# Performance work log

Hardware: AMD Instinct MI355X
Metric: run time of the kernel (lower is better)

## Reference

```python
import jax, jax.numpy as jnp
import numpy as np

B, T, H, K = 4, 1024, 1024, 16
HD = H // K  # head dim
EPS = 1e-5


def _layernorm(x, g, b):
    mu = jnp.mean(x, axis=-1, keepdims=True)
    var = jnp.mean(jnp.square(x - mu), axis=-1, keepdims=True)
    return (x - mu) * jax.lax.rsqrt(var + EPS) * g + b


def setup_inputs() -> dict:
    key = jax.random.key(0)
    ks = jax.random.split(key, 16)
    s = 0.02
    return {
        "x": jax.random.normal(ks[0], (B, T, H), jnp.float32),
        "ln1_g": jnp.ones((H,), jnp.float32),
        "ln1_b": jnp.zeros((H,), jnp.float32),
        "ln2_g": jnp.ones((H,), jnp.float32),
        "ln2_b": jnp.zeros((H,), jnp.float32),
        "Wq": jax.random.normal(ks[1], (H, H), jnp.float32) * s,
        "bq": jnp.zeros((H,), jnp.float32),
        "Wk": jax.random.normal(ks[2], (H, H), jnp.float32) * s,
        "bk": jnp.zeros((H,), jnp.float32),
        "Wv": jax.random.normal(ks[3], (H, H), jnp.float32) * s,
        "bv": jnp.zeros((H,), jnp.float32),
        "W1": jax.random.normal(ks[4], (H, 4 * H), jnp.float32) * s,
        "b1": jnp.zeros((4 * H,), jnp.float32),
        "W2": jax.random.normal(ks[5], (4 * H, H), jnp.float32) * s,
        "b2": jnp.zeros((H,), jnp.float32),
    }


def reference(x, ln1_g, ln1_b, ln2_g, ln2_b, Wq, bq, Wk, bk, Wv, bv, W1, b1, W2, b2):
    # --- attention sub-block ---
    h = _layernorm(x, ln1_g, ln1_b)                      # (B,T,H)
    q = (h @ Wq + bq).reshape(B, T, K, HD).transpose(0, 2, 1, 3)  # (B,K,T,hd)
    k = (h @ Wk + bk).reshape(B, T, K, HD).transpose(0, 2, 1, 3)
    v = (h @ Wv + bv).reshape(B, T, K, HD).transpose(0, 2, 1, 3)
    qkt = jnp.einsum('bkqd,bkpd->bkqp', q, k)            # (B,K,T,T)
    attn = qkt * (1.0 / np.sqrt(HD))
    # module quirk: masked positions are FILLED with 1e-9 (not -inf) before softmax
    causal_mask = jnp.triu(jnp.ones((T, T), bool), k=1)  # True above diagonal = masked
    attn = jnp.where(causal_mask, jnp.float32(1e-9), attn)
    attn = jax.nn.softmax(attn, axis=-1)
    y = jnp.einsum('bkqp,bkpd->bkqd', attn, v)           # (B,K,T,hd)
    y = y.transpose(0, 2, 1, 3).reshape(B, T, H)
    x = x + y
    # --- MLP sub-block (dropout is identity at eval) ---
    h2 = _layernorm(x, ln2_g, ln2_b)
    m = jax.nn.gelu(h2 @ W1 + b1, approximate=False) @ W2 + b2
    return x + m
```

## Files before the change

kernel.cpp:

```cpp
#include <hip/hip_runtime.h>
#include <hip/hip_bf16.h>
#include <math.h>


typedef __attribute__((ext_vector_type(8))) short bf16x8;
typedef __attribute__((ext_vector_type(4))) float f32x4;

#define DEVINL __device__ __forceinline__

#define LOG2E_SCALE 0.18033688f
#define MASK2 1.4426950408889634e-9f

DEVINL void stage16(const __hip_bfloat16* g, short* l) {
  __builtin_amdgcn_global_load_lds(
      (const __attribute__((address_space(1))) unsigned int*)g,
      (__attribute__((address_space(3))) unsigned int*)l, 16, 0, 0);
}

DEVINL float bf2f(short u) {
  unsigned x = ((unsigned)(unsigned short)u) << 16;
  float f; __builtin_memcpy(&f, &x, 4); return f;
}

DEVINL short f2bf_s(float f) {
  __hip_bfloat16 h = __float2bfloat16(f);
  short s; __builtin_memcpy(&s, &h, 2); return s;
}

DEVINL float block_sum(float v, float* sb) {
  #pragma unroll
  for (int o = 32; o; o >>= 1) v += __shfl_down(v, o);
  const int lane = threadIdx.x & 63, w = threadIdx.x >> 6;
  if (lane == 0) sb[w] = v;
  __syncthreads();
  float r = sb[0] + sb[1] + sb[2] + sb[3];
  __syncthreads();
  return r;
}

template<int BM, int BN, int WM, int WN>
DEVINL void gemm_core64(const __hip_bfloat16* __restrict__ A, int lda,
                        const __hip_bfloat16* __restrict__ Bt, int ldb,
                        int Kd, int row0, int col0,
                        f32x4 (&acc)[WM/16][WN/16],
                        short* lds_a, short* lds_b) {
  constexpr int MI = WM / 16, NI = WN / 16, WNC = BN / WN;
  constexpr int CA = BM * 8, CB = BN * 8;
  const int tid = threadIdx.x;
  const int lane = tid & 63, wave = tid >> 6;
  const int wm = (wave / WNC) * WM, wn = (wave % WNC) * WN;
  const int lr = lane & 15, lq = lane >> 4;
  for (int k0 = 0; k0 < Kd; k0 += 64) {
    #pragma unroll
    for (int c = tid; c < CA; c += 256) {
      const int r = c >> 3, kc = ((c & 7) ^ (r & 7)) << 3;
      stage16(A + (size_t)(row0 + r) * lda + k0 + kc, lds_a + c * 8);
    }
    #pragma unroll
    for (int c = tid; c < CB; c += 256) {
      const int r = c >> 3, kc = ((c & 7) ^ (r & 7)) << 3;
      stage16(Bt + (size_t)(col0 + r) * ldb + k0 + kc, lds_b + c * 8);
    }
    __syncthreads();
    #pragma unroll
    for (int s = 0; s < 2; s++) {
      bf16x8 af[MI], bfr[NI];
      #pragma unroll
      for (int mi = 0; mi < MI; mi++) {
        const int m = wm + mi * 16 + lr;
        af[mi] = *(const bf16x8*)(lds_a + m * 64 + (((s * 4 + lq) ^ (m & 7)) << 3));
      }
      #pragma unroll
      for (int ni = 0; ni < NI; ni++) {
        const int n = wn + ni * 16 + lr;
        bfr[ni] = *(const bf16x8*)(lds_b + n * 64 + (((s * 4 + lq) ^ (n & 7)) << 3));
      }
      #pragma unroll
      for (int mi = 0; mi < MI; mi++)
        #pragma unroll
        for (int ni = 0; ni < NI; ni++)
          acc[mi][ni] = __builtin_amdgcn_mfma_f32_16x16x32_bf16(
              af[mi], bfr[ni], acc[mi][ni], 0, 0, 0);
    }
    __syncthreads();
  }
}

__global__ __launch_bounds__(256) void k_tcvt(const float* __restrict__ src,
                                              __hip_bfloat16* __restrict__ dst,
                                              int R, int C, int dstOff, int dstPitch) {
  __shared__ float tile[32][33];
  const int c0 = blockIdx.x * 32, r0 = blockIdx.y * 32;
  const int tx = threadIdx.x, ty = threadIdx.y;
  #pragma unroll
  for (int i = 0; i < 32; i += 8)
    tile[ty + i][tx] = src[(size_t)(r0 + ty + i) * C + c0 + tx];
  __syncthreads();
  #pragma unroll
  for (int i = 0; i < 32; i += 8)
    dst[(size_t)(c0 + ty + i + dstOff) * dstPitch + r0 + tx] =
        __float2bfloat16(tile[tx][ty + i]);
}

__global__ __launch_bounds__(256) void k_tcvt3(const float* __restrict__ Wq,
                                               const float* __restrict__ Wk,
                                               const float* __restrict__ Wv,
                                               __hip_bfloat16* __restrict__ dst) {
  __shared__ float tile[32][33];
  const float* src = blockIdx.z == 0 ? Wq : (blockIdx.z == 1 ? Wk : Wv);
  const int dstOff = blockIdx.z << 10;
  const int c0 = blockIdx.x * 32, r0 = blockIdx.y * 32;
  const int tx = threadIdx.x, ty = threadIdx.y;
  #pragma unroll
  for (int i = 0; i < 32; i += 8)
    tile[ty + i][tx] = src[(size_t)(r0 + ty + i) * 1024 + c0 + tx];
  __syncthreads();
  #pragma unroll
  for (int i = 0; i < 32; i += 8)
    dst[(size_t)(c0 + ty + i + dstOff) * 1024 + r0 + tx] =
        __float2bfloat16(tile[tx][ty + i]);
}

__global__ __launch_bounds__(256) void k_pack_bias(const float* __restrict__ bq,
                                                   const float* __restrict__ bk,
                                                   const float* __restrict__ bv,
                                                   float* __restrict__ o) {
  const int i = blockIdx.x * 256 + threadIdx.x;
  if (i < 3072)
    o[i] = i < 1024 ? bq[i] : (i < 2048 ? bk[i - 1024] : bv[i - 2048]);
}

__global__ __launch_bounds__(256) void k_ln(const float* __restrict__ x,
                                            const float* __restrict__ y,
                                            const float* __restrict__ g,
                                            const float* __restrict__ bb,
                                            __hip_bfloat16* __restrict__ o,
                                            const float* __restrict__ badd,
                                            float* __restrict__ oinit) {
  __shared__ float sb[4];
  const int t = threadIdx.x;
  const size_t base = (size_t)blockIdx.x * 1024 + t * 4;
  const int c = t * 4;
  float4 xv = *(const float4*)(x + base);
  if (y) {
    float4 yv = *(const float4*)(y + base);
    xv.x += yv.x; xv.y += yv.y; xv.z += yv.z; xv.w += yv.w;
    float4 ov;
    ov.x = xv.x + badd[c + 0]; ov.y = xv.y + badd[c + 1];
    ov.z = xv.z + badd[c + 2]; ov.w = xv.w + badd[c + 3];
    *(float4*)(oinit + base) = ov;
  }
  const float mu = block_sum(xv.x + xv.y + xv.z + xv.w, sb) * (1.f / 1024.f);
  const float dx = xv.x - mu, dy = xv.y - mu, dz = xv.z - mu, dw = xv.w - mu;
  const float var = block_sum(dx * dx + dy * dy + dz * dz + dw * dw, sb) * (1.f / 1024.f);
  const float rs = rsqrtf(var + 1e-5f);
  o[base + 0] = __float2bfloat16(dx * rs * g[c + 0] + bb[c + 0]);
  o[base + 1] = __float2bfloat16(dy * rs * g[c + 1] + bb[c + 1]);
  o[base + 2] = __float2bfloat16(dz * rs * g[c + 2] + bb[c + 2]);
  o[base + 3] = __float2bfloat16(dw * rs * g[c + 3] + bb[c + 3]);
}

__global__ __launch_bounds__(256) void k_gemm_qkv(
    const __hip_bfloat16* __restrict__ h1, const __hip_bfloat16* __restrict__ Wt,
    const float* __restrict__ bqkv, __hip_bfloat16* __restrict__ Q,
    __hip_bfloat16* __restrict__ K, __hip_bfloat16* __restrict__ Vt) {
  __shared__ alignas(16) short smem[16896];
  short* la = smem;
  short* lb = smem + 8192;
  short* lc = smem;
  const int row0 = blockIdx.x * 128, col0 = blockIdx.y * 128;
  f32x4 acc[4][4] = {};
  gemm_core64<128, 128, 64, 64>(h1, 1024, Wt, 1024, 1024, row0, col0, acc, la, lb);
  const int tid = threadIdx.x, lane = tid & 63, wave = tid >> 6;
  const int wm = (wave >> 1) * 64, wn = (wave & 1) * 64, lr = lane & 15, lq = lane >> 4;
  const int which = col0 >> 10;
  const int h0 = (col0 & 1023) >> 6;
  const int b = row0 >> 10, t0 = row0 & 1023;
  if (which < 2) {
    const float qs = (which == 0) ? LOG2E_SCALE : 1.f;
    #pragma unroll
    for (int mi = 0; mi < 4; mi++)
      #pragma unroll
      for (int ni = 0; ni < 4; ni++)
        #pragma unroll
        for (int r = 0; r < 4; r++) {
          const int row = wm + mi * 16 + lq * 4 + r;
          const int col = wn + ni * 16 + lr;
          lc[row * 132 + col] = f2bf_s((acc[mi][ni][r] + bqkv[col0 + col]) * qs);
        }
    __syncthreads();
    __hip_bfloat16* O = which == 0 ? Q : K;
    #pragma unroll
    for (int c = 0; c < 8; c++) {
      const int f = tid + 256 * c;
      const int r = f >> 4, cc = f & 15;
      const int col = cc * 8;
      const int head = h0 + (col >> 6), d = col & 63;
      float4 vv = *(const float4*)(lc + r * 132 + col);
      *(float4*)(O + (((size_t)(b * 16 + head)) << 16) + (t0 + r) * 64 + d) = vv;
    }
  } else {
    #pragma unroll
    for (int mi = 0; mi < 4; mi++)
      #pragma unroll
      for (int ni = 0; ni < 4; ni++)
        #pragma unroll
        for (int r = 0; r < 4; r++) {
          const int row = wm + mi * 16 + lq * 4 + r;
          const int col = wn + ni * 16 + lr;
          lc[col * 132 + row] = f2bf_s(acc[mi][ni][r] + bqkv[col0 + col]);
        }
    __syncthreads();
    #pragma unroll
    for (int c = 0; c < 8; c++) {
      const int f = tid + 256 * c;
      const int dl = f >> 4, tc = f & 15;
      const int head = h0 + (dl >> 6), d = dl & 63;
      float4 vv = *(const float4*)(lc + dl * 132 + tc * 8);
      *(float4*)(Vt + (((size_t)(b * 16 + head)) << 16) + (size_t)d * 1024 +
                 t0 + tc * 8) = vv;
    }
  }
}

__global__ __launch_bounds__(256) void k_tailv(const __hip_bfloat16* __restrict__ Vt,
                                               float* __restrict__ TV) {
  __shared__ float ts[8][64];
  const int hb = blockIdx.x, tid = threadIdx.x;
  const __hip_bfloat16* Vh = Vt + ((size_t)hb << 16);
  for (int w = tid; w < 512; w += 256) {
    const int kt = w >> 6, d = w & 63;
    const short* p = (const short*)(Vh + (size_t)d * 1024 + kt * 128);
    float s = 0.f;
    for (int j = 0; j < 128; j += 8) {
      bf16x8 v = *(const bf16x8*)(p + j);
      #pragma unroll
      for (int e = 0; e < 8; e++) s += bf2f(v[e]);
    }
    ts[kt][d] = s;
  }
  __syncthreads();
  for (int w = tid; w < 512; w += 256) {
    const int qt = w >> 6, d = w & 63;
    float s = 0.f;
    for (int kt = qt + 1; kt < 8; kt++) s += ts[kt][d];
    TV[((size_t)hb * 8 + qt) * 64 + d] = s;
  }
}

__global__ __launch_bounds__(256, 3) void k_attn(
    const __hip_bfloat16* __restrict__ Q, const __hip_bfloat16* __restrict__ K,
    const __hip_bfloat16* __restrict__ Vt, const float* __restrict__ TV,
    float* __restrict__ y) {
  __shared__ short lp[64 * 130];
  __shared__ short lK[128 * 64];
  __shared__ short lV[128 * 64];
  const int hb = blockIdx.y;
  const int j = (blockIdx.y & 32) ? (15 - (int)blockIdx.x) : (int)blockIdx.x;
  const int q0 = j * 64;
  const int nkt = (j >> 1) + 1;
  const int tid = threadIdx.x, lane = tid & 63, wave = tid >> 6;
  const int lr = lane & 15, lq = lane >> 4;
  const int wm = wave * 16;
  const __hip_bfloat16* Qh = Q + ((size_t)hb << 16);
  const __hip_bfloat16* Kh = K + ((size_t)hb << 16);
  const __hip_bfloat16* Vh = Vt + ((size_t)hb << 16);

  bf16x8 qf[2];
  #pragma unroll
  for (int s = 0; s < 2; s++)
    qf[s] = *(const bf16x8*)((const short*)Qh +
                             (size_t)(q0 + wm + lr) * 64 + s * 32 + lq * 8);

  f32x4 oacc[4] = {};
  float mrow[4], lrow[4];
  #pragma unroll
  for (int r = 0; r < 4; r++) { mrow[r] = -1e30f; lrow[r] = 0.f; }

  for (int c = tid; c < 1024; c += 256)
    stage16(Kh + (size_t)(c >> 3) * 64 + (((c & 7) ^ ((c >> 3) & 7)) << 3),
            lK + c * 8);
  __syncthreads();

  for (int kt = 0; kt < nkt; kt++) {
    const int k0 = kt * 128;
    f32x4 sacc[8] = {};
    __builtin_amdgcn_s_setprio(1);
    #pragma unroll
    for (int s = 0; s < 2; s++) {
      bf16x8 bf[8];
      #pragma unroll
      for (int ni = 0; ni < 8; ni++) {
        const int n = ni * 16 + lr;
        bf[ni] = *(const bf16x8*)(lK + n * 64 + (((s * 4 + lq) ^ (n & 7)) << 3));
      }
      #pragma unroll
      for (int ni = 0; ni < 8; ni++)
        sacc[ni] = __builtin_amdgcn_mfma_f32_16x16x32_bf16(
            qf[s], bf[ni], sacc[ni], 0, 0, 0);
    }
    __builtin_amdgcn_s_setprio(0);
    __syncthreads();
    for (int c = tid; c < 1024; c += 256)
      stage16(Vh + (size_t)(c >> 4) * 1024 + k0 + (((c & 15) ^ ((c >> 4) & 15)) << 3),
              lV + c * 8);
    if (kt + 1 < nkt) {
      const int k1 = k0 + 128;
      for (int c = tid; c < 1024; c += 256)
        stage16(Kh + (size_t)(k1 + (c >> 3)) * 64 + (((c & 7) ^ ((c >> 3) & 7)) << 3),
                lK + c * 8);
    }
    const bool last = (kt == nkt - 1);
    #pragma unroll
    for (int r = 0; r < 4; r++) {
      const int grow = q0 + wm + lq * 4 + r;
      float tmax = -1e30f;
      #pragma unroll
      for (int ni = 0; ni < 8; ni++) {
        float v = sacc[ni][r];
        if (last && (k0 + ni * 16 + lr) > grow) v = MASK2;
        sacc[ni][r] = v;
        tmax = fmaxf(tmax, v);
      }
      #pragma unroll
      for (int msk = 8; msk; msk >>= 1) tmax = fmaxf(tmax, __shfl_xor(tmax, msk));
      const float mn = fmaxf(mrow[r], tmax);
      const float al = __builtin_amdgcn_exp2f(mrow[r] - mn);
      float rs = 0.f;
      #pragma unroll
      for (int ni = 0; ni < 8; ni++) {
        const float pv = __builtin_amdgcn_exp2f(sacc[ni][r] - mn);
        sacc[ni][r] = pv;
        rs += pv;
      }
      #pragma unroll
      for (int msk = 8; msk; msk >>= 1) rs += __shfl_xor(rs, msk);
      mrow[r] = mn;
      lrow[r] = lrow[r] * al + rs;
      #pragma unroll
      for (int ni = 0; ni < 4; ni++) oacc[ni][r] *= al;
    }
    #pragma unroll
    for (int r = 0; r < 4; r++) {
      const int row = wm + lq * 4 + r;
      #pragma unroll
      for (int ni = 0; ni < 8; ni++)
        lp[row * 130 + ni * 16 + lr] = f2bf_s(sacc[ni][r]);
    }
    __syncthreads();
    __builtin_amdgcn_s_setprio(1);
    #pragma unroll
    for (int ks = 0; ks < 4; ks++) {
      bf16x8 pa, vb[4];
      pa = *(const bf16x8*)(lp + (wm + lr) * 130 + ks * 32 + lq * 8);
      #pragma unroll
      for (int ni = 0; ni < 4; ni++) {
        const int d = ni * 16 + lr;
        vb[ni] = *(const bf16x8*)(lV + d * 128 + (((ks * 4 + lq) ^ (d & 15)) << 3));
      }
      #pragma unroll
      for (int ni = 0; ni < 4; ni++)
        oacc[ni] = __builtin_amdgcn_mfma_f32_16x16x32_bf16(
            pa, vb[ni], oacc[ni], 0, 0, 0);
    }
    __builtin_amdgcn_s_setprio(0);
  }

  const int b = hb >> 4, h = hb & 15;
  const float cv = (float)(1024 - nkt * 128);
  const float* tv = TV + ((size_t)hb * 8 + (j >> 1)) * 64;
  #pragma unroll
  for (int r = 0; r < 4; r++) {
    const int t = q0 + wm + lq * 4 + r;
    const float tail = __builtin_amdgcn_exp2f(MASK2 - mrow[r]);
    const float inv = 1.f / (lrow[r] + cv * tail);
    #pragma unroll
    for (int ni = 0; ni < 4; ni++) {
      const int d = ni * 16 + lr;
      y[((size_t)(b * 1024 + t) << 10) + h * 64 + d] =
          (oacc[ni][r] + tail * tv[d]) * inv;
    }
  }
}

__global__ __launch_bounds__(512, 2) void k_gemm_mlp1(const __hip_bfloat16* __restrict__ h2,
                                                      const __hip_bfloat16* __restrict__ W1t,
                                                      const float* __restrict__ b1,
                                                      __hip_bfloat16* __restrict__ G) {
  __shared__ alignas(16) short smem[32768];
  const int row0 = blockIdx.x * 256, col0 = blockIdx.y * 256;
  const int tid = threadIdx.x, lane = tid & 63, wid = tid >> 6;
  const int lr = lane & 15, lq = lane >> 4;
  const int wm = (wid >> 2) * 128, wn = (wid & 3) * 64;
  const __hip_bfloat16* A = h2 + (size_t)row0 * 1024;
  const __hip_bfloat16* Bt = W1t + (size_t)col0 * 1024;

  auto STAGE = [&](const __hip_bfloat16* src, int k0, short* dst) {
    #pragma unroll
    for (int i = 0; i < 2; i++) {
      const int f = tid + i * 512;
      const int u = f >> 3, P = f & 7, Gc = P ^ (u & 7);
      const int r = u * 2 + (Gc >> 2), g = Gc & 3;
      stage16(src + (size_t)r * 1024 + k0 + g * 8, dst + f * 8);
    }
  };

  f32x4 acc[8][4] = {};
  STAGE(A, 0, smem);
  STAGE(Bt, 0, smem + 16384);
  for (int t = 0; t < 32; ++t) {
    const int cur = t & 1;
    short* pa = smem + cur * 8192;
    short* pb = smem + 16384 + cur * 8192;
    if (t + 1 < 32) {
      short* na = smem + (cur ^ 1) * 8192;
      short* nb = smem + 16384 + (cur ^ 1) * 8192;
      STAGE(A, (t + 1) * 32, na);
      STAGE(Bt, (t + 1) * 32, nb);
      asm volatile("s_waitcnt vmcnt(4)" ::: "memory");
    } else {
      asm volatile("s_waitcnt vmcnt(0)" ::: "memory");
    }
    asm volatile("s_barrier" ::: "memory");
    bf16x8 af[8], bfr[4];
    #pragma unroll
    for (int mi = 0; mi < 8; mi++) {
      const int r = wm + mi * 16 + lr;
      af[mi] = *(const bf16x8*)(pa + (r >> 1) * 64 +
                ((((((r & 1) << 2) | lq)) ^ ((r >> 1) & 7)) << 3));
    }
    #pragma unroll
    for (int ni = 0; ni < 4; ni++) {
      const int n = wn + ni * 16 + lr;
      bfr[ni] = *(const bf16x8*)(pb + (n >> 1) * 64 +
                ((((((n & 1) << 2) | lq)) ^ ((n >> 1) & 7)) << 3));
    }
    __builtin_amdgcn_s_setprio(1);
    #pragma unroll
    for (int mi = 0; mi < 8; mi++)
      #pragma unroll
      for (int ni = 0; ni < 4; ni++)
        acc[mi][ni] = __builtin_amdgcn_mfma_f32_16x16x32_bf16(
            af[mi], bfr[ni], acc[mi][ni], 0, 0, 0);
    __builtin_amdgcn_s_setprio(0);
    asm volatile("s_barrier" ::: "memory");
  }

  short* lc = smem;
  #pragma unroll
  for (int pr = 0; pr < 4; pr++) {
    if ((wid >> 2) == (pr >> 1)) {
      const int mib = (pr & 1) * 4;
      #pragma unroll
      for (int mi2 = 0; mi2 < 4; mi2++)
        #pragma unroll
        for (int ni = 0; ni < 4; ni++)
          #pragma unroll
          for (int rr = 0; rr < 4; rr++) {
            const int rloc = mi2 * 16 + lq * 4 + rr;
            const int col = wn + ni * 16 + lr;
            float v = acc[mib + mi2][ni][rr] + b1[col0 + col];
            const float u2 = fminf(v * (2.3022079f + 0.1029434f * v * v), 80.f);
            const float e = __builtin_amdgcn_exp2f(u2);
            v = v * e * __builtin_amdgcn_rcpf(e + 1.f);
            lc[rloc * 264 + col] = f2bf_s(v);
          }
    }
    __syncthreads();
    #pragma unroll
    for (int c = 0; c < 4; c++) {
      const int f = tid + 512 * c;
      const int r = f >> 5, cc = f & 31;
      float4 vv = *(const float4*)(lc + r * 264 + cc * 8);
      *(float4*)(G + ((size_t)(row0 + pr * 64 + r) << 12) + col0 + cc * 8) = vv;
    }
    __syncthreads();
  }
}

__global__ __launch_bounds__(256) void k_gemm_mlp2(const __hip_bfloat16* __restrict__ G,
                                                   const __hip_bfloat16* __restrict__ W2t,
                                                   float* __restrict__ out) {
  __shared__ alignas(16) short smem[12288];
  short* la = smem;
  short* lb = smem + 8192;
  const int row0 = blockIdx.x * 128, col0 = blockIdx.y * 64;
  const int kOff = blockIdx.z * 2048;
  f32x4 acc[4][2] = {};
  gemm_core64<128, 64, 64, 32>(G + kOff, 4096, W2t + kOff, 4096, 2048,
                               row0, col0, acc, la, lb);
  const int lane = threadIdx.x & 63, wave = threadIdx.x >> 6;
  const int wm = (wave >> 1) * 64, wn = (wave & 1) * 32, lr = lane & 15, lq = lane >> 4;
  #pragma unroll
  for (int mi = 0; mi < 4; mi++)
    #pragma unroll
    for (int ni = 0; ni < 2; ni++)
      #pragma unroll
      for (int r = 0; r < 4; r++) {
        const int grow = row0 + wm + mi * 16 + lq * 4 + r;
        const int gcol = col0 + wn + ni * 16 + lr;
        atomicAdd(out + (((size_t)grow << 10) + gcol), acc[mi][ni][r]);
      }
}

extern "C" void kernel_launch(void* const* d_in, const int* in_sizes, int n_in,
                              void* d_out, int out_size, void* d_ws, size_t ws_size,
                              hipStream_t stream) {
  const float* x     = (const float*)d_in[0];
  const float* ln1_g = (const float*)d_in[1];
  const float* ln1_b = (const float*)d_in[2];
  const float* ln2_g = (const float*)d_in[3];
  const float* ln2_b = (const float*)d_in[4];
  const float* Wq    = (const float*)d_in[5];
  const float* bq    = (const float*)d_in[6];
  const float* Wk    = (const float*)d_in[7];
  const float* bk    = (const float*)d_in[8];
  const float* Wv    = (const float*)d_in[9];
  const float* bv    = (const float*)d_in[10];
  const float* W1    = (const float*)d_in[11];
  const float* b1    = (const float*)d_in[12];
  const float* W2    = (const float*)d_in[13];
  const float* b2    = (const float*)d_in[14];
  float* out = (float*)d_out;

  char* p = (char*)d_ws;
  auto alloc = [&](size_t bytes) { char* r = p; p += (bytes + 255) & ~(size_t)255; return r; };
  __hip_bfloat16* wqkv = (__hip_bfloat16*)alloc(3072 * 1024 * 2);
  __hip_bfloat16* w1t  = (__hip_bfloat16*)alloc(4096 * 1024 * 2);
  __hip_bfloat16* w2t  = (__hip_bfloat16*)alloc(1024 * 4096 * 2);
  float*          bqkv = (float*)alloc(3072 * 4);
  __hip_bfloat16* h1   = (__hip_bfloat16*)alloc(4096 * 1024 * 2);
  __hip_bfloat16* Qb   = (__hip_bfloat16*)alloc((size_t)64 * 65536 * 2);
  __hip_bfloat16* Kb   = (__hip_bfloat16*)alloc((size_t)64 * 65536 * 2);
  __hip_bfloat16* Vt   = (__hip_bfloat16*)alloc((size_t)64 * 65536 * 2);
  float*          TV   = (float*)alloc((size_t)64 * 8 * 64 * 4);
  float*          yb   = (float*)alloc((size_t)4096 * 1024 * 4);
  __hip_bfloat16* h2   = (__hip_bfloat16*)alloc(4096 * 1024 * 2);
  __hip_bfloat16* G    = (__hip_bfloat16*)alloc((size_t)4096 * 4096 * 2);
  (void)ws_size; (void)in_sizes; (void)n_in; (void)out_size;

  const dim3 b256(256), bt(32, 8);
  k_tcvt3<<<dim3(32, 32, 3), bt, 0, stream>>>(Wq, Wk, Wv, wqkv);
  k_tcvt<<<dim3(128, 32), bt, 0, stream>>>(W1, w1t, 1024, 4096, 0, 1024);
  k_tcvt<<<dim3(32, 128), bt, 0, stream>>>(W2, w2t, 4096, 1024, 0, 4096);
  k_pack_bias<<<12, b256, 0, stream>>>(bq, bk, bv, bqkv);

  k_ln<<<4096, b256, 0, stream>>>(x, nullptr, ln1_g, ln1_b, h1, nullptr, nullptr);
  k_gemm_qkv<<<dim3(32, 24), b256, 0, stream>>>(h1, wqkv, bqkv, Qb, Kb, Vt);
  k_tailv<<<64, b256, 0, stream>>>(Vt, TV);
  k_attn<<<dim3(16, 64), b256, 0, stream>>>(Qb, Kb, Vt, TV, yb);

  k_ln<<<4096, b256, 0, stream>>>(x, yb, ln2_g, ln2_b, h2, b2, out);
  k_gemm_mlp1<<<dim3(16, 16), dim3(512), 0, stream>>>(h2, w1t, b1, G);
  k_gemm_mlp2<<<dim3(32, 16, 2), b256, 0, stream>>>(G, w2t, out);
}
```

Measured before the change: 332.8 us.

## Restructure MLP1 GEMM into 8-phase pipeline with K=64 tiles and split staging

Rewrites the main loop of the first MLP GEMM to use K=64 tiles in two double-buffered halves (even/odd) and splits each iteration into eight phases. Each phase interleaves an LDS fragment read, a half-tile global-to-LDS stage, a barrier, and a block of MFMAs. The aim is finer overlap of global loads and LDS reads with matrix math, plus fewer barriers per unit of K work. It doubles shared memory to 128 KB per block, which with two blocks per CU may limit occupancy, and it adds more fine-grained barriers and waitcnt coordination.

After: 329.6 us. About the same (-0.9%).

```diff
diff --git a/kernel.cpp b/kernel.cpp
--- a/kernel.cpp
+++ b/kernel.cpp
@@ -383,67 +383,129 @@
   }
 }
 
+template<int MH, int NH>
+DEVINL void ph_read(const short* pa, const short* pb, int wr, int wc,
+                    int lr, int lq, bf16x8 (&af)[4][2], bf16x8 (&bf)[2][2]) {
+  if (NH == 0) {
+    #pragma unroll
+    for (int mi2 = 0; mi2 < 4; mi2++)
+      #pragma unroll
+      for (int ks = 0; ks < 2; ks++) {
+        const int r = wr * 128 + MH * 64 + mi2 * 16 + lr;
+        af[mi2][ks] = *(const bf16x8*)(pa + r * 64 + (((ks * 4 + lq) ^ (r & 7)) << 3));
+      }
+  }
+  #pragma unroll
+  for (int ni2 = 0; ni2 < 2; ni2++)
+    #pragma unroll
+    for (int ks = 0; ks < 2; ks++) {
+      const int n = wc * 64 + NH * 32 + ni2 * 16 + lr;
+      bf[ni2][ks] = *(const bf16x8*)(pb + n * 64 + (((ks * 4 + lq) ^ (n & 7)) << 3));
+    }
+}
+
+DEVINL void ph_sync() {
+  __builtin_amdgcn_s_barrier();
+  asm volatile("s_waitcnt lgkmcnt(0)" ::: "memory");
+  __builtin_amdgcn_sched_barrier(0);
+}
+
+template<int MH, int NH>
+DEVINL void ph_mfma(f32x4 (&acc)[8][4], bf16x8 (&af)[4][2], bf16x8 (&bf)[2][2]) {
+  __builtin_amdgcn_s_setprio(1);
+  #pragma unroll
+  for (int mi2 = 0; mi2 < 4; mi2++)
+    #pragma unroll
+    for (int ni2 = 0; ni2 < 2; ni2++)
+      #pragma unroll
+      for (int ks = 0; ks < 2; ks++)
+        acc[MH * 4 + mi2][NH * 2 + ni2] = __builtin_amdgcn_mfma_f32_16x16x32_bf16(
+            af[mi2][ks], bf[ni2][ks], acc[MH * 4 + mi2][NH * 2 + ni2], 0, 0, 0);
+  __builtin_amdgcn_s_setprio(0);
+  __builtin_amdgcn_s_barrier();
+}
+
 __global__ __launch_bounds__(512, 2) void k_gemm_mlp1(const __hip_bfloat16* __restrict__ h2,
                                                       const __hip_bfloat16* __restrict__ W1t,
                                                       const float* __restrict__ b1,
                                                       __hip_bfloat16* __restrict__ G) {
-  __shared__ alignas(16) short smem[32768];
+  __shared__ alignas(16) short smem[65536];
+  short* Ae = smem;
+  short* Ao = smem + 16384;
+  short* Be = smem + 32768;
+  short* Bo = smem + 49152;
   const int row0 = blockIdx.x * 256, col0 = blockIdx.y * 256;
   const int tid = threadIdx.x, lane = tid & 63, wid = tid >> 6;
   const int lr = lane & 15, lq = lane >> 4;
-  const int wm = (wid >> 2) * 128, wn = (wid & 3) * 64;
+  const int wr = wid >> 2, wc = wid & 3;
   const __hip_bfloat16* A = h2 + (size_t)row0 * 1024;
   const __hip_bfloat16* Bt = W1t + (size_t)col0 * 1024;
 
-  auto STAGE = [&](const __hip_bfloat16* src, int k0, short* dst) {
-    #pragma unroll
-    for (int i = 0; i < 2; i++) {
-      const int f = tid + i * 512;
-      const int u = f >> 3, P = f & 7, Gc = P ^ (u & 7);
-      const int r = u * 2 + (Gc >> 2), g = Gc & 3;
-      stage16(src + (size_t)r * 1024 + k0 + g * 8, dst + f * 8);
+  auto STG = [&](const __hip_bfloat16* src, int k0, int h, short* dst, int SH) {
+    #pragma unroll
+    for (int ii = 0; ii < 2; ii++) {
+      const int f = tid + ii * 512;
+      const int rp = f >> 3, P = f & 7;
+      const int r = ((rp >> SH) << (SH + 1)) | (h << SH) | (rp & ((1 << SH) - 1));
+      const int g = P ^ (r & 7);
+      stage16(src + (size_t)r * 1024 + k0 + g * 8, dst + r * 64 + P * 8);
     }
   };
 
   f32x4 acc[8][4] = {};
-  STAGE(A, 0, smem);
-  STAGE(Bt, 0, smem + 16384);
-  for (int t = 0; t < 32; ++t) {
-    const int cur = t & 1;
-    short* pa = smem + cur * 8192;
-    short* pb = smem + 16384 + cur * 8192;
-    if (t + 1 < 32) {
-      short* na = smem + (cur ^ 1) * 8192;
-      short* nb = smem + 16384 + (cur ^ 1) * 8192;
-      STAGE(A, (t + 1) * 32, na);
-      STAGE(Bt, (t + 1) * 32, nb);
+  bf16x8 af[4][2], bf[2][2];
+
+  STG(A, 0, 0, Ae, 6);  STG(Bt, 0, 0, Be, 5);
+  STG(A, 0, 1, Ae, 6);  STG(Bt, 0, 1, Be, 5);
+  STG(A, 64, 0, Ao, 6); STG(Bt, 64, 0, Bo, 5);
+  asm volatile("s_waitcnt vmcnt(4)" ::: "memory");
+  __syncthreads();
+
+  for (int i = 0; i < 8; ++i) {
+    const int kE1 = (i + 1) * 128;
+    const int kO0 = i * 128 + 64;
+    const int kO1 = kE1 + 64;
+    const bool more = (i + 1 < 8);
+    ph_read<0, 0>(Ae, Be, wr, wc, lr, lq, af, bf);
+    STG(A, kO0, 1, Ao, 6);
+    ph_sync();
+    ph_mfma<0, 0>(acc, af, bf);
+    ph_read<0, 1>(Ae, Be, wr, wc, lr, lq, af, bf);
+    STG(Bt, kO0, 1, Bo, 5);
+    ph_sync();
+    ph_mfma<0, 1>(acc, af, bf);
+    ph_read<1, 0>(Ae, Be, wr, wc, lr, lq, af, bf);
+    if (more) STG(A, kE1, 0, Ae, 6);
+    ph_sync();
+    ph_mfma<1, 0>(acc, af, bf);
+    ph_read<1, 1>(Ae, Be, wr, wc, lr, lq, af, bf);
+    if (more) {
+      STG(Bt, kE1, 0, Be, 5);
       asm volatile("s_waitcnt vmcnt(4)" ::: "memory");
     } else {
       asm volatile("s_waitcnt vmcnt(0)" ::: "memory");
     }
-    asm volatile("s_barrier" ::: "memory");
-    bf16x8 af[8], bfr[4];
-    #pragma unroll
-    for (int mi = 0; mi < 8; mi++) {
-      const int r = wm + mi * 16 + lr;
-      af[mi] = *(const bf16x8*)(pa + (r >> 1) * 64 +
-                ((((((r & 1) << 2) | lq)) ^ ((r >> 1) & 7)) << 3));
-    }
-    #pragma unroll
-    for (int ni = 0; ni < 4; ni++) {
-      const int n = wn + ni * 16 + lr;
-      bfr[ni] = *(const bf16x8*)(pb + (n >> 1) * 64 +
-                ((((((n & 1) << 2) | lq)) ^ ((n >> 1) & 7)) << 3));
-    }
-    __builtin_amdgcn_s_setprio(1);
-    #pragma unroll
-    for (int mi = 0; mi < 8; mi++)
-      #pragma unroll
-      for (int ni = 0; ni < 4; ni++)
-        acc[mi][ni] = __builtin_amdgcn_mfma_f32_16x16x32_bf16(
-            af[mi], bfr[ni], acc[mi][ni], 0, 0, 0);
-    __builtin_amdgcn_s_setprio(0);
-    asm volatile("s_barrier" ::: "memory");
+    ph_sync();
+    ph_mfma<1, 1>(acc, af, bf);
+    ph_read<0, 0>(Ao, Bo, wr, wc, lr, lq, af, bf);
+    if (more) STG(A, kE1, 1, Ae, 6);
+    ph_sync();
+    ph_mfma<0, 0>(acc, af, bf);
+    ph_read<0, 1>(Ao, Bo, wr, wc, lr, lq, af, bf);
+    if (more) STG(Bt, kE1, 1, Be, 5);
+    ph_sync();
+    ph_mfma<0, 1>(acc, af, bf);
+    ph_read<1, 0>(Ao, Bo, wr, wc, lr, lq, af, bf);
+    if (more) STG(A, kO1, 0, Ao, 6);
+    ph_sync();
+    ph_mfma<1, 0>(acc, af, bf);
+    ph_read<1, 1>(Ao, Bo, wr, wc, lr, lq, af, bf);
+    if (more) {
+      STG(Bt, kO1, 0, Bo, 5);
+      asm volatile("s_waitcnt vmcnt(4)" ::: "memory");
+    }
+    ph_sync();
+    ph_mfma<1, 1>(acc, af, bf);
   }
 
   short* lc = smem;
@@ -458,7 +520,7 @@
           #pragma unroll
           for (int rr = 0; rr < 4; rr++) {
             const int rloc = mi2 * 16 + lq * 4 + rr;
-            const int col = wn + ni * 16 + lr;
+            const int col = (wid & 3) * 64 + ni * 16 + lr;
             float v = acc[mib + mi2][ni][rr] + b1[col0 + col];
             const float u2 = fminf(v * (2.3022079f + 0.1029434f * v * v), 80.f);
             const float e = __builtin_amdgcn_exp2f(u2);
```
